# Performance work log

Hardware: AMD Instinct MI355X
Metric: run time of the kernel (lower is better)

Reference implementation:

```python
import jax, jax.numpy as jnp
import numpy as np

B, S, D, H = 2, 2048, 1024, 16
DH = D // H


def setup_inputs() -> dict:
    key = jax.random.key(0)
    ks = jax.random.split(key, 12)
    std = 1.0 / np.sqrt(D)
    inp = {
        "q": jax.random.normal(ks[0], (B, S, D), jnp.float32),
        "k": jax.random.normal(ks[1], (B, S, D), jnp.float32),
        "v": jax.random.normal(ks[2], (B, S, D), jnp.float32),
        "mask": jnp.tril(jnp.ones((S, S), jnp.bool_))[None, None],  # causal [1,1,S,S]
        "wq_w": jax.random.uniform(ks[3], (D, D), jnp.float32, -std, std),
        "wq_b": jax.random.uniform(ks[4], (D,), jnp.float32, -std, std),
        "wk_w": jax.random.uniform(ks[5], (D, D), jnp.float32, -std, std),
        "wk_b": jax.random.uniform(ks[6], (D,), jnp.float32, -std, std),
        "wv_w": jax.random.uniform(ks[7], (D, D), jnp.float32, -std, std),
        "wv_b": jax.random.uniform(ks[8], (D,), jnp.float32, -std, std),
        "wo_w": jax.random.uniform(ks[9], (D, D), jnp.float32, -std, std),
        "wo_b": jax.random.uniform(ks[10], (D,), jnp.float32, -std, std),
    }
    return inp


def reference(q, k, v, mask, wq_w, wq_b, wk_w, wk_b, wv_w, wv_b, wo_w, wo_b):
    b, s, d = q.shape
    dh = d // H
    scale = jnp.sqrt(jnp.asarray(dh, q.dtype))  # scale = d_model/n_heads = d_head

    def proj(x, w, bias):
        y = x @ w.T + bias
        return y.reshape(b, -1, H, dh).transpose(0, 2, 1, 3)  # [B,H,S,dh]

    Q = proj(q, wq_w, wq_b)
    K = proj(k, wk_w, wk_b)
    V = proj(v, wv_w, wv_b)

    score = jnp.einsum("bhqd,bhkd->bhqk", Q, K) / scale
    score = jnp.where(mask, score, jnp.asarray(-1e10, score.dtype))
    attn = jax.nn.softmax(score, axis=-1)
    # dropout is identity in eval mode
    y = jnp.einsum("bhqk,bhkd->bhqd", attn, V)
    y = y.transpose(0, 2, 1, 3).reshape(b, -1, d)
    y = y @ wo_w.T + wo_b
    return y, attn
```

## Files before the change

kernel.cpp:

```cpp
#include <hip/hip_runtime.h>
#include <cstdint>

#define S_LEN   2048
#define D_MODEL 1024
#define NHEAD   16
#define DHEAD   64
#define BATCH   2
#define M_ROWS  (BATCH * S_LEN)

typedef __attribute__((ext_vector_type(8))) short bf16x8;
typedef __attribute__((ext_vector_type(4))) float f32x4;

__device__ __forceinline__ unsigned short f2bf(float f) {
    union { float f; uint32_t u; } v; v.f = f;
    uint32_t u = v.u;
    return (unsigned short)((u + 0x7FFFu + ((u >> 16) & 1u)) >> 16);
}

__device__ __forceinline__ float bf2f(uint32_t u16) {
    union { uint32_t u; float f; } x; x.u = u16 << 16; return x.f;
}

__device__ __forceinline__ uint32_t cvt_pk_bf16(float a, float b) {
    uint32_t r;
    asm("v_cvt_pk_bf16_f32 %0, %1, %2" : "=v"(r) : "v"(a), "v"(b));
    return r;
}

__device__ __forceinline__ void gload_lds16(const void* g, void* l) {
    __builtin_amdgcn_global_load_lds(
        (const __attribute__((address_space(1))) void*)g,
        (__attribute__((address_space(3))) void*)l, 16, 0, 0);
}

struct CvtArgs {
    const float* src[7];
    unsigned short* dst[7];
    int n4[7];
};
__global__ __launch_bounds__(256) void cvt_all(CvtArgs a) {
    const int which = blockIdx.y;
    const int t = blockIdx.x * 256 + threadIdx.x;
    if (t >= a.n4[which]) return;
    f32x4 v = reinterpret_cast<const f32x4*>(a.src[which])[t];
    uint2 o;
    o.x = cvt_pk_bf16(v[0], v[1]);
    o.y = cvt_pk_bf16(v[2], v[3]);
    reinterpret_cast<uint2*>(a.dst[which])[t] = o;
}

template<int MODE>
__device__ __forceinline__ void gemm_body(
    unsigned short* lA, unsigned short* lB,
    const unsigned short* __restrict__ A,
    const unsigned short* __restrict__ Bw,
    const float* __restrict__ bias,
    void* __restrict__ Cout,
    int bx, int by, float prescale)
{
    constexpr int K = 1024;
    const int tid  = threadIdx.x;
    const int lane = tid & 63;
    const int w    = tid >> 6;
    const int wr   = w >> 1, wc = w & 1;
    const int g    = lane >> 4, r16 = lane & 15;
    const int brow = by * 128;
    const int bcol = bx * 128;

    f32x4 acc[4][4];
#pragma unroll
    for (int i = 0; i < 4; ++i)
#pragma unroll
        for (int j = 0; j < 4; ++j) acc[i][j] = (f32x4){0.f, 0.f, 0.f, 0.f};

    const int rA0 = tid >> 2;
    const int cc  = (tid & 3) * 8;

    for (int kk = 0; kk < K; kk += 32) {
#pragma unroll
        for (int it = 0; it < 2; ++it) {
            int r = it * 64 + rA0;
            gload_lds16(A  + (size_t)(brow + r) * K + kk + cc, &lA[r * 32 + cc]);
            gload_lds16(Bw + (size_t)(bcol + r) * K + kk + cc, &lB[r * 32 + cc]);
        }
        __syncthreads();
        bf16x8 af[4], bfr[4];
#pragma unroll
        for (int i = 0; i < 4; ++i)
            af[i] = *reinterpret_cast<const bf16x8*>(&lA[(wr * 64 + i * 16 + r16) * 32 + g * 8]);
#pragma unroll
        for (int j = 0; j < 4; ++j)
            bfr[j] = *reinterpret_cast<const bf16x8*>(&lB[(wc * 64 + j * 16 + r16) * 32 + g * 8]);
#pragma unroll
        for (int i = 0; i < 4; ++i)
#pragma unroll
            for (int j = 0; j < 4; ++j)
                acc[i][j] = __builtin_amdgcn_mfma_f32_16x16x32_bf16(af[i], bfr[j], acc[i][j], 0, 0, 0);
        __syncthreads();
    }

#pragma unroll
    for (int i = 0; i < 4; ++i) {
#pragma unroll
        for (int j = 0; j < 4; ++j) {
            const int n = bcol + wc * 64 + j * 16 + r16;
#pragma unroll
            for (int rr = 0; rr < 4; ++rr) {
                const int m = brow + wr * 64 + i * 16 + g * 4 + rr;
                float val = acc[i][j][rr];
                if (MODE == 0) {
                    val = (val + bias[n]) * prescale;
                    int b = m >> 11, s = m & 2047;
                    int h = n >> 6,  d = n & 63;
                    ((unsigned short*)Cout)[(((size_t)(b * NHEAD + h)) * S_LEN + s) * DHEAD + d] = f2bf(val);
                } else if (MODE == 1) {
                    val += bias[m];
                    int h = m >> 6,  d = m & 63;
                    int b = n >> 11, s = n & 2047;
                    ((unsigned short*)Cout)[(((size_t)(b * NHEAD + h)) * DHEAD + d) * S_LEN + s] = f2bf(val);
                } else {
                    val += bias[n];
                    ((float*)Cout)[(size_t)m * D_MODEL + n] = val;
                }
            }
        }
    }
}

__global__ __launch_bounds__(256) void proj_all(
    const unsigned short* qb, const unsigned short* wqb, const float* wq_b, unsigned short* Qhp,
    const unsigned short* kb, const unsigned short* wkb, const float* wk_b, unsigned short* Khp,
    const unsigned short* vb, const unsigned short* wvb, const float* wv_b, unsigned short* Vtp,
    float qscale)
{
    __shared__ unsigned short lA[128 * 32];
    __shared__ unsigned short lB[128 * 32];
    const int bid = blockIdx.x;
    const int z = bid >> 8, t = bid & 255;
    if (z == 0)
        gemm_body<0>(lA, lB, qb, wqb, wq_b, Qhp, t & 7, t >> 3, qscale);
    else if (z == 1)
        gemm_body<0>(lA, lB, kb, wkb, wk_b, Khp, t & 7, t >> 3, 1.0f);
    else
        gemm_body<1>(lA, lB, wvb, vb, wv_b, Vtp, t & 31, t >> 5, 1.0f);
}

__global__ __launch_bounds__(512, 2) void attn_ctx_kernel(
    const unsigned short* __restrict__ Qh,
    const unsigned short* __restrict__ Kh,
    const unsigned short* __restrict__ Vt,
    float* __restrict__ stats,
    unsigned short* __restrict__ ctx)
{
    __shared__ unsigned short ldsK[2][64 * 64];
    __shared__ unsigned short ldsV[2][64 * 64];
    __shared__ unsigned short pS[8][16 * 72];

    const int tid  = threadIdx.x;
    const int lane = tid & 63;
    const int w    = tid >> 6;
    const int g    = lane >> 4, r16 = lane & 15;
    const int wg   = w & 3;
    const int grp  = w >> 2;

    const int lid = blockIdx.x;
    const int xcd = lid & 7;
    const int rest = lid >> 3;
    const int bh  = xcd * 4 + (rest >> 3);
    const int ii  = rest & 7;
    const int b   = bh >> 4, h = bh & 15;

    const unsigned short* Kp = Kh + (size_t)bh * S_LEN * DHEAD;
    const unsigned short* Vp = Vt + (size_t)bh * DHEAD * S_LEN;

    const int srow = tid >> 3;
    const int scol = (tid & 7) * 16;
    const int sswz = scol ^ ((srow & 7) << 4);
    const int rsw  = (r16 & 7) << 4;

    unsigned short* pl = pS[w];

    for (int pp = 0; pp < 2; ++pp) {
        const int p  = pp == 0 ? ii : 15 - ii;
        const int qh = 16 + p;
        const int ql = 15 - p;
        const int qtile = grp == 0 ? qh : ql;
        const int qw    = qtile * 64 + wg * 16;
        const int qrel  = wg * 16 + r16;
        const int myN   = qtile;

        const unsigned short* Qp = Qh + ((size_t)bh * S_LEN + qw) * DHEAD;
        bf16x8 qf[2];
#pragma unroll
        for (int d2 = 0; d2 < 2; ++d2)
            qf[d2] = *reinterpret_cast<const bf16x8*>(Qp + (size_t)r16 * DHEAD + d2 * 32 + g * 8);

        auto stageKV = [&](int kt, int buf) {
            gload_lds16((const char*)Kp + (size_t)(kt * 64 + srow) * 128 + sswz,
                        (char*)ldsK[buf] + tid * 16);
            gload_lds16((const char*)Vp + (size_t)srow * (S_LEN * 2) + (size_t)kt * 128 + sswz,
                        (char*)ldsV[buf] + tid * 16);
        };

        float l_run = 0.f;
        f32x4 of[4];
#pragma unroll
        for (int nt = 0; nt < 4; ++nt) of[nt] = (f32x4){0, 0, 0, 0};

        int buf = 0;
        stageKV(0, 0);
        __syncthreads();
        for (int t = 0; t <= qh; ++t) {
            if (t < qh) stageKV(t + 1, buf ^ 1);
            if (t <= myN) {
                const bool masked = (t == myN);
                bf16x8 kf[8];
#pragma unroll
                for (int d2 = 0; d2 < 2; ++d2)
#pragma unroll
                    for (int nt = 0; nt < 4; ++nt)
                        kf[d2 * 4 + nt] = *reinterpret_cast<const bf16x8*>(
                            (const char*)ldsK[buf] + (nt * 16 + r16) * 128 + ((d2 * 64 + g * 16) ^ rsw));
                f32x4 sf[4];
#pragma unroll
                for (int nt = 0; nt < 4; ++nt) sf[nt] = (f32x4){0, 0, 0, 0};
                __builtin_amdgcn_s_setprio(1);
#pragma unroll
                for (int d2 = 0; d2 < 2; ++d2)
#pragma unroll
                    for (int nt = 0; nt < 4; ++nt)
                        sf[nt] = __builtin_amdgcn_mfma_f32_16x16x32_bf16(kf[d2 * 4 + nt], qf[d2], sf[nt], 0, 0, 0);
                __builtin_amdgcn_s_setprio(0);
                float sum = 0.f;
#pragma unroll
                for (int nt = 0; nt < 4; ++nt)
#pragma unroll
                    for (int rr = 0; rr < 4; ++rr) {
                        float e = __builtin_amdgcn_exp2f(sf[nt][rr]);
                        if (masked && (nt * 16 + g * 4 + rr > qrel)) e = 0.f;
                        sf[nt][rr] = e;
                        sum += e;
                    }
                l_run += sum;
#pragma unroll
                for (int nt = 0; nt < 4; ++nt) {
                    uint2 pk2;
                    pk2.x = cvt_pk_bf16(sf[nt][0], sf[nt][1]);
                    pk2.y = cvt_pk_bf16(sf[nt][2], sf[nt][3]);
                    *reinterpret_cast<uint2*>(&pl[r16 * 72 + nt * 16 + g * 4]) = pk2;
                }
                __builtin_amdgcn_wave_barrier();
                __builtin_amdgcn_s_setprio(1);
#pragma unroll
                for (int kh = 0; kh < 2; ++kh) {
                    bf16x8 pa = *reinterpret_cast<const bf16x8*>(&pl[r16 * 72 + kh * 32 + g * 8]);
#pragma unroll
                    for (int nt = 0; nt < 4; ++nt) {
                        bf16x8 vf = *reinterpret_cast<const bf16x8*>(
                            (const char*)ldsV[buf] + (nt * 16 + r16) * 128 + ((kh * 64 + g * 16) ^ rsw));
                        of[nt] = __builtin_amdgcn_mfma_f32_16x16x32_bf16(vf, pa, of[nt], 0, 0, 0);
                    }
                }
                __builtin_amdgcn_s_setprio(0);
            }
            __syncthreads();
            buf ^= 1;
        }

        float lx = l_run;
        lx += __shfl_xor(lx, 16);
        lx += __shfl_xor(lx, 32);
        const float mprime = __builtin_amdgcn_logf(lx);
        if (lane < 16)
            stats[(size_t)bh * S_LEN + qw + r16] = mprime;

        const float inv = 1.f / lx;
        const size_t crow = ((size_t)b * S_LEN + qw + r16) * D_MODEL + h * DHEAD;
#pragma unroll
        for (int nt = 0; nt < 4; ++nt) {
            uint2 pk2;
            pk2.x = cvt_pk_bf16(of[nt][0] * inv, of[nt][1] * inv);
            pk2.y = cvt_pk_bf16(of[nt][2] * inv, of[nt][3] * inv);
            *reinterpret_cast<uint2*>(&ctx[crow + nt * 16 + g * 4]) = pk2;
        }
        __syncthreads();
    }
}

__global__ __launch_bounds__(256) void fused_out(
    const unsigned short* __restrict__ ctx,
    const unsigned short* __restrict__ wob,
    const float* __restrict__ wo_b,
    float* __restrict__ yout,
    const unsigned short* __restrict__ Qh,
    const unsigned short* __restrict__ Kh,
    const float* __restrict__ stats,
    float* __restrict__ attn_out)
{
    __shared__ unsigned short lds[128 * 32 * 2];
    const int bid = blockIdx.x;
    if (bid < 256) {
        gemm_body<2>(lds, lds + 128 * 32, ctx, wob, wo_b, yout, bid & 7, bid >> 3, 1.0f);
        return;
    }

    const int tid  = threadIdx.x;
    const int lane = tid & 63;
    const int w    = tid >> 6;
    const int g    = lane >> 4, r16 = lane & 15;
    const int rl   = lane >> 4;
    const int c4   = (lane & 15) * 4;

    const int pid = bid - 256;
    const int xcd = pid & 7;
    const int rest = pid >> 3;
    const int bh  = xcd * 4 + (rest >> 5);
    const int qt  = rest & 31;

    const int qw   = qt * 64 + w * 16;
    const int qrel = w * 16 + r16;
    float* rowbase = attn_out + (size_t)bh * S_LEN * S_LEN + (size_t)qw * S_LEN;

    const unsigned short* Qp = Qh + ((size_t)bh * S_LEN + qw) * DHEAD;
    const unsigned short* Kp = Kh + (size_t)bh * S_LEN * DHEAD;

    bf16x8 qf[2];
#pragma unroll
    for (int d2 = 0; d2 < 2; ++d2)
        qf[d2] = *reinterpret_cast<const bf16x8*>(Qp + (size_t)r16 * DHEAD + d2 * 32 + g * 8);
    const float mpr = stats[(size_t)bh * S_LEN + qw + r16];

    unsigned short* pl = lds + w * (16 * 72);

    for (int kt = 0; kt <= qt; ++kt) {
        bf16x8 kf[8];
#pragma unroll
        for (int d2 = 0; d2 < 2; ++d2)
#pragma unroll
            for (int nt = 0; nt < 4; ++nt)
                kf[d2 * 4 + nt] = *reinterpret_cast<const bf16x8*>(
                    Kp + (size_t)(kt * 64 + nt * 16 + r16) * DHEAD + d2 * 32 + g * 8);
        f32x4 sf[4];
#pragma unroll
        for (int nt = 0; nt < 4; ++nt) sf[nt] = (f32x4){0, 0, 0, 0};
        __builtin_amdgcn_s_setprio(1);
#pragma unroll
        for (int d2 = 0; d2 < 2; ++d2)
#pragma unroll
            for (int nt = 0; nt < 4; ++nt)
                sf[nt] = __builtin_amdgcn_mfma_f32_16x16x32_bf16(kf[d2 * 4 + nt], qf[d2], sf[nt], 0, 0, 0);
        __builtin_amdgcn_s_setprio(0);

        const bool masked = (kt == qt);
#pragma unroll
        for (int nt = 0; nt < 4; ++nt) {
#pragma unroll
            for (int rr = 0; rr < 4; ++rr) {
                float p = __builtin_amdgcn_exp2f(sf[nt][rr] - mpr);
                if (masked && (nt * 16 + g * 4 + rr > qrel)) p = 0.f;
                sf[nt][rr] = p;
            }
            uint2 pk2;
            pk2.x = cvt_pk_bf16(sf[nt][0], sf[nt][1]);
            pk2.y = cvt_pk_bf16(sf[nt][2], sf[nt][3]);
            *reinterpret_cast<uint2*>(&pl[r16 * 72 + nt * 16 + g * 4]) = pk2;
        }
        __builtin_amdgcn_wave_barrier();
        float* dst0 = rowbase + kt * 64;
#pragma unroll
        for (int i = 0; i < 4; ++i) {
            const int r = i * 4 + rl;
            uint2 dpk = *reinterpret_cast<const uint2*>(&pl[r * 72 + c4]);
            f32x4 o;
            o[0] = bf2f(dpk.x & 0xffffu);
            o[1] = bf2f(dpk.x >> 16);
            o[2] = bf2f(dpk.y & 0xffffu);
            o[3] = bf2f(dpk.y >> 16);
            __builtin_nontemporal_store(o, reinterpret_cast<f32x4*>(dst0 + (size_t)r * S_LEN + c4));
        }
        __builtin_amdgcn_wave_barrier();
    }

    const int z0 = (qt + 1) * 64;
    const f32x4 z4 = (f32x4){0.f, 0.f, 0.f, 0.f};
    for (int r = 0; r < 16; ++r) {
        float* dst = rowbase + (size_t)r * S_LEN;
        for (int c = z0 + lane * 4; c < S_LEN; c += 256)
            __builtin_nontemporal_store(z4, reinterpret_cast<f32x4*>(dst + c));
    }
}

extern "C" void kernel_launch(void* const* d_in, const int* in_sizes, int n_in,
                              void* d_out, int out_size, void* d_ws, size_t ws_size,
                              hipStream_t stream)
{
    const float* q    = (const float*)d_in[0];
    const float* k    = (const float*)d_in[1];
    const float* v    = (const float*)d_in[2];
    const float* wq_w = (const float*)d_in[4];
    const float* wq_b = (const float*)d_in[5];
    const float* wk_w = (const float*)d_in[6];
    const float* wk_b = (const float*)d_in[7];
    const float* wv_w = (const float*)d_in[8];
    const float* wv_b = (const float*)d_in[9];
    const float* wo_w = (const float*)d_in[10];
    const float* wo_b = (const float*)d_in[11];

    char* ws = (char*)d_ws;
    const size_t MB = 1024 * 1024;
    unsigned short* qb  = (unsigned short*)(ws + 0 * MB);
    unsigned short* kb  = (unsigned short*)(ws + 8 * MB);
    unsigned short* vb  = (unsigned short*)(ws + 16 * MB);
    unsigned short* wqb = (unsigned short*)(ws + 24 * MB);
    unsigned short* wkb = (unsigned short*)(ws + 26 * MB);
    unsigned short* wvb = (unsigned short*)(ws + 28 * MB);
    unsigned short* wob = (unsigned short*)(ws + 30 * MB);
    unsigned short* Qhp = (unsigned short*)(ws + 32 * MB);
    unsigned short* Khp = (unsigned short*)(ws + 40 * MB);
    unsigned short* Vtp = (unsigned short*)(ws + 48 * MB);
    unsigned short* ctx = (unsigned short*)(ws + 56 * MB);
    float* stats = (float*)(ws + 0 * MB);

    float* yout = (float*)d_out;
    float* attn = yout + (size_t)M_ROWS * D_MODEL;

    CvtArgs ca;
    ca.src[0] = q;    ca.dst[0] = qb;  ca.n4[0] = M_ROWS * D_MODEL / 4;
    ca.src[1] = k;    ca.dst[1] = kb;  ca.n4[1] = M_ROWS * D_MODEL / 4;
    ca.src[2] = v;    ca.dst[2] = vb;  ca.n4[2] = M_ROWS * D_MODEL / 4;
    ca.src[3] = wq_w; ca.dst[3] = wqb; ca.n4[3] = D_MODEL * D_MODEL / 4;
    ca.src[4] = wk_w; ca.dst[4] = wkb; ca.n4[4] = D_MODEL * D_MODEL / 4;
    ca.src[5] = wv_w; ca.dst[5] = wvb; ca.n4[5] = D_MODEL * D_MODEL / 4;
    ca.src[6] = wo_w; ca.dst[6] = wob; ca.n4[6] = D_MODEL * D_MODEL / 4;
    cvt_all<<<dim3((M_ROWS * D_MODEL / 4 + 255) / 256, 7), dim3(256), 0, stream>>>(ca);

    const float qscale = 0.125f * 1.44269504088896340736f;
    proj_all<<<dim3(768), dim3(256), 0, stream>>>(
        qb, wqb, wq_b, Qhp,
        kb, wkb, wk_b, Khp,
        vb, wvb, wv_b, Vtp, qscale);

    attn_ctx_kernel<<<dim3(256), dim3(512), 0, stream>>>(Qhp, Khp, Vtp, stats, ctx);

    fused_out<<<dim3(256 + 1024), dim3(256), 0, stream>>>(
        ctx, wob, wo_b, yout, Qhp, Khp, stats, attn);
}
```

Measured before the change: 253.3 us.

## Split attention-probability writeback into balanced 64x128 tiles with transposed zero fill

```diff
diff --git a/kernel.cpp b/kernel.cpp
--- a/kernel.cpp
+++ b/kernel.cpp
@@ -297,7 +297,7 @@
     const float* __restrict__ stats,
     float* __restrict__ attn_out)
 {
-    __shared__ unsigned short lds[128 * 32 * 2];
+    __shared__ unsigned short lds[64 * 136 + 64];
     const int bid = blockIdx.x;
     if (bid < 256) {
         gemm_body<2>(lds, lds + 128 * 32, ctx, wob, wo_b, yout, bid & 7, bid >> 3, 1.0f);
@@ -313,14 +313,35 @@
 
     const int pid = bid - 256;
     const int xcd = pid & 7;
-    const int rest = pid >> 3;
-    const int bh  = xcd * 4 + (rest >> 5);
-    const int qt  = rest & 31;
+    const int cid = pid >> 3;
+    const int bh  = xcd * 4 + cid / 272;
+    const int t   = cid % 272;
+    int m = (int)((sqrtf(4.f * t + 1.f) - 1.f) * 0.5f);
+    while (m * (m + 1) > t) --m;
+    while ((m + 1) * (m + 2) <= t) ++m;
+    int qt, c2;
+    if (t < (m + 1) * (m + 1)) { qt = 2 * m;     c2 = t - m * (m + 1); }
+    else                       { qt = 2 * m + 1; c2 = t - (m + 1) * (m + 1); }
+
+    float* abase = attn_out + (size_t)bh * S_LEN * S_LEN;
+
+    const f32x4 z4 = (f32x4){0.f, 0.f, 0.f, 0.f};
+#pragma unroll
+    for (int s = 0; s < 2; ++s) {
+        const int tr = 2 * c2 + s;
+        if (qt > tr) {
+            float* dstZ = abase + (size_t)(tr * 64) * S_LEN + qt * 64;
+#pragma unroll
+            for (int i = 0; i < 4; ++i) {
+                const int r = w * 16 + i * 4 + rl;
+                __builtin_nontemporal_store(z4,
+                    reinterpret_cast<f32x4*>(dstZ + (size_t)r * S_LEN + c4));
+            }
+        }
+    }
 
     const int qw   = qt * 64 + w * 16;
     const int qrel = w * 16 + r16;
-    float* rowbase = attn_out + (size_t)bh * S_LEN * S_LEN + (size_t)qw * S_LEN;
-
     const unsigned short* Qp = Qh + ((size_t)bh * S_LEN + qw) * DHEAD;
     const unsigned short* Kp = Kh + (size_t)bh * S_LEN * DHEAD;
 
@@ -330,9 +351,18 @@
         qf[d2] = *reinterpret_cast<const bf16x8*>(Qp + (size_t)r16 * DHEAD + d2 * 32 + g * 8);
     const float mpr = stats[(size_t)bh * S_LEN + qw + r16];
 
-    unsigned short* pl = lds + w * (16 * 72);
-
-    for (int kt = 0; kt <= qt; ++kt) {
+    unsigned short* plw = lds + w * (16 * 136);
+
+#pragma unroll
+    for (int kl = 0; kl < 2; ++kl) {
+        const int kt = 2 * c2 + kl;
+        if (kt > qt) {
+            const uint2 zz = {0u, 0u};
+#pragma unroll
+            for (int nt = 0; nt < 4; ++nt)
+                *reinterpret_cast<uint2*>(&plw[r16 * 136 + kl * 64 + nt * 16 + g * 4]) = zz;
+            continue;
+        }
         bf16x8 kf[8];
 #pragma unroll
         for (int d2 = 0; d2 < 2; ++d2)
@@ -350,7 +380,6 @@
             for (int nt = 0; nt < 4; ++nt)
                 sf[nt] = __builtin_amdgcn_mfma_f32_16x16x32_bf16(kf[d2 * 4 + nt], qf[d2], sf[nt], 0, 0, 0);
         __builtin_amdgcn_s_setprio(0);
-
         const bool masked = (kt == qt);
 #pragma unroll
         for (int nt = 0; nt < 4; ++nt) {
@@ -363,30 +392,24 @@
             uint2 pk2;
             pk2.x = cvt_pk_bf16(sf[nt][0], sf[nt][1]);
             pk2.y = cvt_pk_bf16(sf[nt][2], sf[nt][3]);
-            *reinterpret_cast<uint2*>(&pl[r16 * 72 + nt * 16 + g * 4]) = pk2;
-        }
-        __builtin_amdgcn_wave_barrier();
-        float* dst0 = rowbase + kt * 64;
-#pragma unroll
-        for (int i = 0; i < 4; ++i) {
-            const int r = i * 4 + rl;
-            uint2 dpk = *reinterpret_cast<const uint2*>(&pl[r * 72 + c4]);
-            f32x4 o;
-            o[0] = bf2f(dpk.x & 0xffffu);
-            o[1] = bf2f(dpk.x >> 16);
-            o[2] = bf2f(dpk.y & 0xffffu);
-            o[3] = bf2f(dpk.y >> 16);
-            __builtin_nontemporal_store(o, reinterpret_cast<f32x4*>(dst0 + (size_t)r * S_LEN + c4));
-        }
-        __builtin_amdgcn_wave_barrier();
-    }
-
-    const int z0 = (qt + 1) * 64;
-    const f32x4 z4 = (f32x4){0.f, 0.f, 0.f, 0.f};
-    for (int r = 0; r < 16; ++r) {
-        float* dst = rowbase + (size_t)r * S_LEN;
-        for (int c = z0 + lane * 4; c < S_LEN; c += 256)
-            __builtin_nontemporal_store(z4, reinterpret_cast<f32x4*>(dst + c));
+            *reinterpret_cast<uint2*>(&plw[r16 * 136 + kl * 64 + nt * 16 + g * 4]) = pk2;
+        }
+    }
+    __builtin_amdgcn_wave_barrier();
+
+    float* dst0 = abase + (size_t)qw * S_LEN + c2 * 128;
+    const int rsub = lane >> 5;
+    const int cc2  = (lane & 31) * 4;
+#pragma unroll
+    for (int i = 0; i < 8; ++i) {
+        const int r = i * 2 + rsub;
+        uint2 d = *reinterpret_cast<const uint2*>(&plw[r * 136 + cc2]);
+        f32x4 o;
+        o[0] = bf2f(d.x & 0xffffu);
+        o[1] = bf2f(d.x >> 16);
+        o[2] = bf2f(d.y & 0xffffu);
+        o[3] = bf2f(d.y >> 16);
+        __builtin_nontemporal_store(o, reinterpret_cast<f32x4*>(dst0 + (size_t)r * S_LEN + cc2));
     }
 }
 
@@ -442,6 +465,6 @@
 
     attn_ctx_kernel<<<dim3(256), dim3(512), 0, stream>>>(Qhp, Khp, Vtp, stats, ctx);
 
-    fused_out<<<dim3(256 + 1024), dim3(256), 0, stream>>>(
+    fused_out<<<dim3(256 + 8704), dim3(256), 0, stream>>>(
         ctx, wob, wo_b, yout, Qhp, Khp, stats, attn);
 }
```

Result: faster. 227.2 us (-10.3%).
